# Kernel optimization log

Measured on AMD Instinct MI355X. Metric: run time of the kernel, lower is better.

The kernel has to match this reference:

```python
import jax, jax.numpy as jnp
import numpy as np

N_COMPRESS = 512
N_EXPAND_QK = 512
N_EXPAND_V = 512
TOPK_C, TOPK_QK, TOPK_V = 8, 4, 6


def setup_inputs() -> dict:
    key = jax.random.key(0)
    k1, k2, k3 = jax.random.split(key, 3)
    B, S, D, DS = 4, 4096, 2048, 64
    N = N_COMPRESS + N_EXPAND_QK + N_EXPAND_V
    x = jax.random.normal(k1, (B, S, D), dtype=jnp.float32)
    importance = jax.random.uniform(k2, (B, S), dtype=jnp.float32)
    W_proj = jax.random.normal(k3, (D, DS), dtype=jnp.float32) * (1.0 / np.sqrt(D))
    b_proj = jnp.zeros((DS,), dtype=jnp.float32)
    neuron_emb = jax.random.normal(jax.random.fold_in(key, 7), (N, DS), dtype=jnp.float32) * 0.02
    return {"x": x, "importance": importance, "W_proj": W_proj, "b_proj": b_proj, "neuron_emb": neuron_emb}


def _topk_sparsify(w, k):
    # w: [B, N]; keep top-k per row, zero the rest, renormalize (matches torch scatter path)
    vals, idx = jax.lax.top_k(w, k)
    B = w.shape[0]
    sparse = jnp.zeros_like(w).at[jnp.arange(B)[:, None], idx].set(vals)
    return sparse / (sparse.sum(axis=-1, keepdims=True) + 1e-8)


def reference(x, importance, W_proj, b_proj, neuron_emb):
    # token projection into unified neuron space
    h = x @ W_proj + b_proj                              # [B, S, d_space]
    emb_n = neuron_emb / jnp.maximum(
        jnp.linalg.norm(neuron_emb, axis=-1, keepdims=True), 1e-12)
    all_logits = jnp.einsum('bsd,nd->bsn', h, emb_n)     # [B, S, N_total]

    c_end = N_COMPRESS
    qk_end = N_COMPRESS + N_EXPAND_QK
    compress_pref = jax.nn.softmax(all_logits[..., :c_end], axis=-1)
    pref_QK = jax.nn.softmax(all_logits[..., c_end:qk_end], axis=-1)  # Q and K share logits (eval mode)
    pref_V = jax.nn.softmax(all_logits[..., qk_end:], axis=-1)

    # importance-weighted pooling over the sequence
    dense_C = jnp.einsum('bs,bsn->bn', importance, compress_pref)
    dense_QK = jnp.einsum('bs,bsn->bn', importance, pref_QK)
    dense_V = jnp.einsum('bs,bsn->bn', importance, pref_V)

    w_C = _topk_sparsify(dense_C, TOPK_C)
    w_Q = _topk_sparsify(dense_QK, TOPK_QK)
    w_K = _topk_sparsify(dense_QK, TOPK_QK)
    w_V = _topk_sparsify(dense_V, TOPK_V)
    return jnp.stack([w_C, w_Q, w_K, w_V], axis=0)       # [4, B, N_group]
```

## Files before the change

### kernel.cpp

```cpp
#include <hip/hip_runtime.h>

#define NTOT 1536
#define DD 2048
#define BB 4
#define SS 4096
#define NBB 42
#define TPB 98
#define NTILE 7

typedef __attribute__((ext_vector_type(8))) short bf16x8;
typedef __attribute__((ext_vector_type(4))) float f32x4;

__device__ __forceinline__ void split1(float v, unsigned short& hi, unsigned short& lo) {
  unsigned u = __float_as_uint(v);
  hi = (unsigned short)(u >> 16);
  float hf = __uint_as_float(u & 0xffff0000u);
  float r = v - hf;
  lo = (unsigned short)(__float_as_uint(r) >> 16);
}

__global__ __launch_bounds__(256) void k_prep_emb(const float* __restrict__ emb,
                                                  short* __restrict__ eH,
                                                  short* __restrict__ eL) {
  int wave = threadIdx.x >> 6;
  int lane = threadIdx.x & 63;
  int n = blockIdx.x * 4 + wave;
  float v = emb[n * 64 + lane];
  float ss = v * v;
#pragma unroll
  for (int off = 32; off; off >>= 1) ss += __shfl_xor(ss, off, 64);
  float nrm = fmaxf(sqrtf(ss), 1e-12f);
  float nv = v / nrm;
  unsigned short hi, lo;
  split1(nv, hi, lo);
  eH[n * 64 + lane] = (short)hi;
  eL[n * 64 + lane] = (short)lo;
}

__global__ __launch_bounds__(256) void k_prepw(const float* __restrict__ W,
                                               short* __restrict__ imgH,
                                               short* __restrict__ imgL) {
  int kt = blockIdx.x;
  for (int idx = threadIdx.x; idx < 4096; idx += 256) {
    int n = idx & 63;
    int q = idx >> 6;
    int p = q >> 3;
    int e = q & 7;
    int s = p ^ (n & 7);
    int k = kt * 64 + s * 8 + e;
    float v = W[k * 64 + n];
    unsigned short hi, lo;
    split1(v, hi, lo);
    int flat = kt * 4096 + n * 64 + p * 8 + e;
    imgH[flat] = (short)hi;
    imgL[flat] = (short)lo;
  }
}

__device__ __forceinline__ void split8(float4 a, float4 b, bf16x8& hi, bf16x8& lo) {
  float v[8] = {a.x, a.y, a.z, a.w, b.x, b.y, b.z, b.w};
#pragma unroll
  for (int i = 0; i < 8; ++i) {
    unsigned u = __float_as_uint(v[i]);
    hi[i] = (short)(u >> 16);
    float hf = __uint_as_float(u & 0xffff0000u);
    float r = v[i] - hf;
    lo[i] = (short)(__float_as_uint(r) >> 16);
  }
}

__global__ __launch_bounds__(128, 3) void k_proj(const float* __restrict__ x,
                                                 const float* __restrict__ imgHf,
                                                 const float* __restrict__ imgLf,
                                                 const float* __restrict__ bias,
                                                 short* __restrict__ hH,
                                                 short* __restrict__ hL) {
  __shared__ float XAs[2][2048];
  __shared__ short BHs[2][4096];
  __shared__ short BLs[2][4096];

  int tid = threadIdx.x;
  int w = tid >> 6;
  int l = tid & 63;
  size_t t0 = (size_t)blockIdx.x * 32;

  int stok = tid >> 4;
  int sslot = tid & 15;

  float4 xr[4], bhr[4], blr[4];
  f32x4 acc[4];
#pragma unroll
  for (int i = 0; i < 4; ++i) acc[i] = (f32x4){0.f, 0.f, 0.f, 0.f};

  const float4* imgH4 = (const float4*)imgHf;
  const float4* imgL4 = (const float4*)imgLf;

#define LOADT(KT)                                                                  \
  {                                                                                \
    _Pragma("unroll") for (int c = 0; c < 4; ++c) {                                \
      int tok = c * 8 + stok;                                                      \
      xr[c] = *(const float4*)(x + (t0 + tok) * DD + (KT) * 64 + sslot * 4);       \
      bhr[c] = imgH4[(KT) * 512 + c * 128 + tid];                                  \
      blr[c] = imgL4[(KT) * 512 + c * 128 + tid];                                  \
    }                                                                              \
  }

#define WRITET(DB)                                                                 \
  {                                                                                \
    _Pragma("unroll") for (int c = 0; c < 4; ++c) {                                \
      int tok = c * 8 + stok;                                                      \
      *(float4*)(&XAs[DB][tok * 64 + ((sslot ^ (tok & 7)) << 2)]) = xr[c];         \
      *(float4*)(&BHs[DB][c * 1024 + tid * 8]) = bhr[c];                           \
      *(float4*)(&BLs[DB][c * 1024 + tid * 8]) = blr[c];                           \
    }                                                                              \
  }

  LOADT(0);
  WRITET(0);
  __syncthreads();

  int db = 0;
  for (int kt = 0; kt < 32; ++kt) {
    if (kt < 31) LOADT(kt + 1);

    int row = w * 16 + (l & 15);
#pragma unroll
    for (int ks = 0; ks < 2; ++ks) {
      int s0 = ks * 8 + (l >> 4) * 2;
      float4 xa = *(const float4*)(&XAs[db][row * 64 + ((s0 ^ (row & 7)) << 2)]);
      float4 xb = *(const float4*)(&XAs[db][row * 64 + (((s0 + 1) ^ (row & 7)) << 2)]);
      bf16x8 ahi, alo;
      split8(xa, xb, ahi, alo);
#pragma unroll
      for (int nf = 0; nf < 4; ++nf) {
        int n = nf * 16 + (l & 15);
        int p = (ks * 4 + (l >> 4)) ^ (n & 7);
        bf16x8 bh = *(const bf16x8*)(&BHs[db][n * 64 + p * 8]);
        bf16x8 bl = *(const bf16x8*)(&BLs[db][n * 64 + p * 8]);
        acc[nf] = __builtin_amdgcn_mfma_f32_16x16x32_bf16(ahi, bh, acc[nf], 0, 0, 0);
        acc[nf] = __builtin_amdgcn_mfma_f32_16x16x32_bf16(alo, bh, acc[nf], 0, 0, 0);
        acc[nf] = __builtin_amdgcn_mfma_f32_16x16x32_bf16(ahi, bl, acc[nf], 0, 0, 0);
      }
    }

    if (kt < 31) WRITET(db ^ 1);
    __syncthreads();
    db ^= 1;
  }

#pragma unroll
  for (int nf = 0; nf < 4; ++nf) {
    int n = nf * 16 + (l & 15);
    float bv = bias[n];
#pragma unroll
    for (int j = 0; j < 4; ++j) {
      size_t tok = t0 + w * 16 + (l >> 4) * 4 + j;
      float v = acc[nf][j] + bv;
      unsigned short hi, lo;
      split1(v, hi, lo);
      hH[tok * 64 + n] = (short)hi;
      hL[tok * 64 + n] = (short)lo;
    }
  }
#undef LOADT
#undef WRITET
}

__global__ __launch_bounds__(512, 2) void k_pref(const short* __restrict__ hH,
                                                 const short* __restrict__ hL,
                                                 const short* __restrict__ eH,
                                                 const short* __restrict__ eL,
                                                 const float* __restrict__ imp,
                                                 float* __restrict__ partials) {
  int bid = blockIdx.x;
  int g = bid / (BB * NBB);
  int rem = bid % (BB * NBB);
  int b = rem / NBB;
  int nb = rem % NBB;
  int tid = threadIdx.x;
  int w = tid >> 6;
  int l = tid & 63;
  int col = l & 15;
  int q = l >> 4;

  __shared__ short BLs[4 * 2 * 512 * 8];
  __shared__ float zred[2][8][16];

  bf16x8 BH[4][2];
  {
    const short* eHg = eH + ((size_t)(g * 512 + w * 64 + col)) * 64 + q * 8;
    const short* eLg = eL + ((size_t)(g * 512 + w * 64 + col)) * 64 + q * 8;
#pragma unroll
    for (int nf = 0; nf < 4; ++nf) {
#pragma unroll
      for (int ks = 0; ks < 2; ++ks) {
        BH[nf][ks] = *(const bf16x8*)(eHg + nf * 1024 + ks * 32);
        bf16x8 blv = *(const bf16x8*)(eLg + nf * 1024 + ks * 32);
        *(bf16x8*)(&BLs[((nf * 2 + ks) * 512 + tid) * 8]) = blv;
      }
    }
  }
  __syncthreads();

  int s0 = nb * TPB;
  int slim = s0 + TPB; if (slim > SS) slim = SS;
  float wsum[4] = {0.f, 0.f, 0.f, 0.f};
  int par = 0;

#pragma unroll 1
  for (int tile = 0; tile < NTILE; ++tile) {
    int tbase = s0 + tile * 16;
    int arow = tbase + col; if (arow > SS - 1) arow = SS - 1;
    size_t hoff = ((size_t)b * SS + arow) * 64;
    bf16x8 AH0 = *(const bf16x8*)(hH + hoff + q * 8);
    bf16x8 AH1 = *(const bf16x8*)(hH + hoff + 32 + q * 8);
    bf16x8 AL0 = *(const bf16x8*)(hL + hoff + q * 8);
    bf16x8 AL1 = *(const bf16x8*)(hL + hoff + 32 + q * 8);

    f32x4 acc[4];
#pragma unroll
    for (int nf = 0; nf < 4; ++nf) acc[nf] = (f32x4){0.f, 0.f, 0.f, 0.f};
#pragma unroll
    for (int nf = 0; nf < 4; ++nf) {
      bf16x8 bl0 = *(const bf16x8*)(&BLs[((nf * 2 + 0) * 512 + tid) * 8]);
      bf16x8 bl1 = *(const bf16x8*)(&BLs[((nf * 2 + 1) * 512 + tid) * 8]);
      acc[nf] = __builtin_amdgcn_mfma_f32_16x16x32_bf16(AH0, BH[nf][0], acc[nf], 0, 0, 0);
      acc[nf] = __builtin_amdgcn_mfma_f32_16x16x32_bf16(AL0, BH[nf][0], acc[nf], 0, 0, 0);
      acc[nf] = __builtin_amdgcn_mfma_f32_16x16x32_bf16(AH0, bl0, acc[nf], 0, 0, 0);
      acc[nf] = __builtin_amdgcn_mfma_f32_16x16x32_bf16(AH1, BH[nf][1], acc[nf], 0, 0, 0);
      acc[nf] = __builtin_amdgcn_mfma_f32_16x16x32_bf16(AL1, BH[nf][1], acc[nf], 0, 0, 0);
      acc[nf] = __builtin_amdgcn_mfma_f32_16x16x32_bf16(AH1, bl1, acc[nf], 0, 0, 0);
    }

    float zp[4];
#pragma unroll
    for (int j = 0; j < 4; ++j) {
      zp[j] = __expf(acc[0][j]) + __expf(acc[1][j]) +
              __expf(acc[2][j]) + __expf(acc[3][j]);
    }
#pragma unroll
    for (int off = 1; off <= 8; off <<= 1) {
#pragma unroll
      for (int j = 0; j < 4; ++j) zp[j] += __shfl_xor(zp[j], off, 64);
    }
    float zw = (col == 0) ? zp[0] : (col == 1) ? zp[1] : (col == 2) ? zp[2] : zp[3];
    if (col < 4) zred[par][w][q * 4 + col] = zw;
    __syncthreads();
    float r0, r1, r2, r3;
    {
#pragma unroll
      for (int j = 0; j < 4; ++j) {
        int t16 = q * 4 + j;
        float Z = 0.f;
#pragma unroll
        for (int ww = 0; ww < 8; ++ww) Z += zred[par][ww][t16];
        int s = tbase + t16;
        float iv = (s < slim) ? imp[(size_t)b * SS + s] : 0.f;
        float r = iv / Z;
        if (j == 0) r0 = r; else if (j == 1) r1 = r; else if (j == 2) r2 = r; else r3 = r;
      }
    }
#pragma unroll
    for (int nf = 0; nf < 4; ++nf) {
      wsum[nf] += __expf(acc[nf][0]) * r0 + __expf(acc[nf][1]) * r1 +
                  __expf(acc[nf][2]) * r2 + __expf(acc[nf][3]) * r3;
    }
    par ^= 1;
  }

#pragma unroll
  for (int nf = 0; nf < 4; ++nf) {
    wsum[nf] += __shfl_xor(wsum[nf], 16, 64);
    wsum[nf] += __shfl_xor(wsum[nf], 32, 64);
  }
  if (q == 0) {
    size_t base = ((size_t)(g * BB + b) * NBB + nb) * 512 + w * 64;
#pragma unroll
    for (int nf = 0; nf < 4; ++nf) partials[base + nf * 16 + col] = wsum[nf];
  }
}

__global__ __launch_bounds__(512) void k_topk(const float* __restrict__ partials,
                                              float* __restrict__ out) {
  int g = blockIdx.x >> 2;
  int b = blockIdx.x & 3;
  int tid = threadIdx.x;
  int wave = tid >> 6, lane = tid & 63;

  __shared__ float lv[8][8];
  __shared__ int li[8][8];

  float dense = 0.f;
  const float* p = partials + (size_t)(g * BB + b) * NBB * 512 + tid;
  for (int nb = 0; nb < NBB; ++nb) dense += p[nb * 512];

  int K = (g == 0) ? 8 : (g == 1) ? 4 : 6;
  float val = dense;
  float ssum = 0.f;
  int sel = 0;
  for (int it = 0; it < K; ++it) {
    float v = val;
    int idx = tid;
#pragma unroll
    for (int off = 32; off; off >>= 1) {
      float ov = __shfl_xor(v, off, 64);
      int oi = __shfl_xor(idx, off, 64);
      if (ov > v || (ov == v && oi < idx)) { v = ov; idx = oi; }
    }
    if (lane == 0) { lv[wave][0] = v; li[wave][0] = idx; }
    __syncthreads();
    float mv = lv[0][0];
    int mi = li[0][0];
#pragma unroll
    for (int ww = 1; ww < 8; ++ww) {
      float wv2 = lv[ww][0];
      int wi = li[ww][0];
      if (wv2 > mv || (wv2 == mv && wi < mi)) { mv = wv2; mi = wi; }
    }
    ssum += mv;
    if (tid == mi) { sel = 1; val = -3.0e38f; }
    __syncthreads();
  }
  float o = sel ? dense / (ssum + 1e-8f) : 0.f;
  int row = (g == 0) ? 0 : (g == 1) ? 1 : 3;
  out[((size_t)row * BB + b) * 512 + tid] = o;
  if (g == 1) out[((size_t)2 * BB + b) * 512 + tid] = o;
}

extern "C" void kernel_launch(void* const* d_in, const int* in_sizes, int n_in,
                              void* d_out, int out_size, void* d_ws, size_t ws_size,
                              hipStream_t stream) {
  const float* x    = (const float*)d_in[0];
  const float* imp  = (const float*)d_in[1];
  const float* W    = (const float*)d_in[2];
  const float* bias = (const float*)d_in[3];
  const float* emb  = (const float*)d_in[4];
  float* out = (float*)d_out;

  char* ws = (char*)d_ws;
  short* imgH     = (short*)(ws + 0);
  short* imgL     = (short*)(ws + 262144);
  short* eH       = (short*)(ws + 524288);
  short* eL       = (short*)(ws + 720896);
  short* hH       = (short*)(ws + 917504);
  short* hL       = (short*)(ws + 3014656);
  float* partials = (float*)(ws + 5111808);

  hipLaunchKernelGGL(k_prep_emb, dim3(384), dim3(256), 0, stream, emb, eH, eL);
  hipLaunchKernelGGL(k_prepw, dim3(32), dim3(256), 0, stream, W, imgH, imgL);
  hipLaunchKernelGGL(k_proj, dim3(512), dim3(128), 0, stream,
                     x, (const float*)imgH, (const float*)imgL, bias, hH, hL);
  hipLaunchKernelGGL(k_pref, dim3(3 * BB * NBB), dim3(512), 0, stream,
                     hH, hL, eH, eL, imp, partials);
  hipLaunchKernelGGL(k_topk, dim3(12), dim3(512), 0, stream, partials, out);
}
```

Baseline: 95.53 us.

## Merge prep kernels, split proj tile across 4 waves, prefetch A tiles in pref

Fuses the embedding-normalize and weight-split prep kernels into one launch to remove a kernel launch. The projection kernel moves from 128 to 256 threads per block, with each of 4 waves computing a 16x32 quadrant instead of 2 waves doing 16x64 each. This is meant to hide more memory latency while keeping the same 32-token tiles. The pref kernel now loads the next tile's h rows into registers before the current tile's MFMAs, overlapping global loads with compute at the cost of extra registers.

```diff
diff --git a/kernel.cpp b/kernel.cpp
--- a/kernel.cpp
+++ b/kernel.cpp
@@ -19,57 +19,47 @@
   lo = (unsigned short)(__float_as_uint(r) >> 16);
 }
 
-__global__ __launch_bounds__(256) void k_prep_emb(const float* __restrict__ emb,
-                                                  short* __restrict__ eH,
-                                                  short* __restrict__ eL) {
-  int wave = threadIdx.x >> 6;
-  int lane = threadIdx.x & 63;
-  int n = blockIdx.x * 4 + wave;
-  float v = emb[n * 64 + lane];
-  float ss = v * v;
-#pragma unroll
-  for (int off = 32; off; off >>= 1) ss += __shfl_xor(ss, off, 64);
-  float nrm = fmaxf(sqrtf(ss), 1e-12f);
-  float nv = v / nrm;
-  unsigned short hi, lo;
-  split1(nv, hi, lo);
-  eH[n * 64 + lane] = (short)hi;
-  eL[n * 64 + lane] = (short)lo;
-}
-
-__global__ __launch_bounds__(256) void k_prepw(const float* __restrict__ W,
-                                               short* __restrict__ imgH,
-                                               short* __restrict__ imgL) {
-  int kt = blockIdx.x;
-  for (int idx = threadIdx.x; idx < 4096; idx += 256) {
-    int n = idx & 63;
-    int q = idx >> 6;
-    int p = q >> 3;
-    int e = q & 7;
-    int s = p ^ (n & 7);
-    int k = kt * 64 + s * 8 + e;
-    float v = W[k * 64 + n];
+__global__ __launch_bounds__(256) void k_prep(const float* __restrict__ emb,
+                                              const float* __restrict__ W,
+                                              short* __restrict__ eH,
+                                              short* __restrict__ eL,
+                                              short* __restrict__ imgH,
+                                              short* __restrict__ imgL) {
+  int bid = blockIdx.x;
+  if (bid < 384) {
+    int wave = threadIdx.x >> 6;
+    int lane = threadIdx.x & 63;
+    int n = bid * 4 + wave;
+    float v = emb[n * 64 + lane];
+    float ss = v * v;
+#pragma unroll
+    for (int off = 32; off; off >>= 1) ss += __shfl_xor(ss, off, 64);
+    float nrm = fmaxf(sqrtf(ss), 1e-12f);
+    float nv = v / nrm;
     unsigned short hi, lo;
-    split1(v, hi, lo);
-    int flat = kt * 4096 + n * 64 + p * 8 + e;
-    imgH[flat] = (short)hi;
-    imgL[flat] = (short)lo;
-  }
-}
-
-__device__ __forceinline__ void split8(float4 a, float4 b, bf16x8& hi, bf16x8& lo) {
-  float v[8] = {a.x, a.y, a.z, a.w, b.x, b.y, b.z, b.w};
-#pragma unroll
-  for (int i = 0; i < 8; ++i) {
-    unsigned u = __float_as_uint(v[i]);
-    hi[i] = (short)(u >> 16);
-    float hf = __uint_as_float(u & 0xffff0000u);
-    float r = v[i] - hf;
-    lo[i] = (short)(__float_as_uint(r) >> 16);
-  }
-}
-
-__global__ __launch_bounds__(128, 3) void k_proj(const float* __restrict__ x,
+    split1(nv, hi, lo);
+    eH[n * 64 + lane] = (short)hi;
+    eL[n * 64 + lane] = (short)lo;
+  } else {
+    int kt = bid - 384;
+    for (int idx = threadIdx.x; idx < 4096; idx += 256) {
+      int n = idx & 63;
+      int q = idx >> 6;
+      int p = q >> 3;
+      int e = q & 7;
+      int s = p ^ (n & 7);
+      int k = kt * 64 + s * 8 + e;
+      float v = W[k * 64 + n];
+      unsigned short hi, lo;
+      split1(v, hi, lo);
+      int flat = kt * 4096 + n * 64 + p * 8 + e;
+      imgH[flat] = (short)hi;
+      imgL[flat] = (short)lo;
+    }
+  }
+}
+
+__global__ __launch_bounds__(256, 2) void k_proj(const float* __restrict__ x,
                                                  const float* __restrict__ imgHf,
                                                  const float* __restrict__ imgLf,
                                                  const float* __restrict__ bias,
@@ -84,34 +74,37 @@
   int l = tid & 63;
   size_t t0 = (size_t)blockIdx.x * 32;
 
-  int stok = tid >> 4;
+  int ty = tid >> 4;
   int sslot = tid & 15;
 
-  float4 xr[4], bhr[4], blr[4];
-  f32x4 acc[4];
-#pragma unroll
-  for (int i = 0; i < 4; ++i) acc[i] = (f32x4){0.f, 0.f, 0.f, 0.f};
+  int th = (w & 1) * 16;
+  int nh = (w >> 1) * 32;
+
+  float4 xr[2], bhr[2], blr[2];
+  f32x4 acc[2];
+#pragma unroll
+  for (int i = 0; i < 2; ++i) acc[i] = (f32x4){0.f, 0.f, 0.f, 0.f};
 
   const float4* imgH4 = (const float4*)imgHf;
   const float4* imgL4 = (const float4*)imgLf;
 
 #define LOADT(KT)                                                                  \
   {                                                                                \
-    _Pragma("unroll") for (int c = 0; c < 4; ++c) {                                \
-      int tok = c * 8 + stok;                                                      \
+    _Pragma("unroll") for (int c = 0; c < 2; ++c) {                                \
+      int tok = c * 16 + ty;                                                       \
       xr[c] = *(const float4*)(x + (t0 + tok) * DD + (KT) * 64 + sslot * 4);       \
-      bhr[c] = imgH4[(KT) * 512 + c * 128 + tid];                                  \
-      blr[c] = imgL4[(KT) * 512 + c * 128 + tid];                                  \
+      bhr[c] = imgH4[(KT) * 512 + c * 256 + tid];                                  \
+      blr[c] = imgL4[(KT) * 512 + c * 256 + tid];                                  \
     }                                                                              \
   }
 
 #define WRITET(DB)                                                                 \
   {                                                                                \
-    _Pragma("unroll") for (int c = 0; c < 4; ++c) {                                \
-      int tok = c * 8 + stok;                                                      \
+    _Pragma("unroll") for (int c = 0; c < 2; ++c) {                                \
+      int tok = c * 16 + ty;                                                       \
       *(float4*)(&XAs[DB][tok * 64 + ((sslot ^ (tok & 7)) << 2)]) = xr[c];         \
-      *(float4*)(&BHs[DB][c * 1024 + tid * 8]) = bhr[c];                           \
-      *(float4*)(&BLs[DB][c * 1024 + tid * 8]) = blr[c];                           \
+      *(float4*)(&BHs[DB][(c * 256 + tid) * 8]) = bhr[c];                          \
+      *(float4*)(&BLs[DB][(c * 256 + tid) * 8]) = blr[c];                          \
     }                                                                              \
   }
 
@@ -123,17 +116,27 @@
   for (int kt = 0; kt < 32; ++kt) {
     if (kt < 31) LOADT(kt + 1);
 
-    int row = w * 16 + (l & 15);
+    int row = th + (l & 15);
 #pragma unroll
     for (int ks = 0; ks < 2; ++ks) {
       int s0 = ks * 8 + (l >> 4) * 2;
       float4 xa = *(const float4*)(&XAs[db][row * 64 + ((s0 ^ (row & 7)) << 2)]);
       float4 xb = *(const float4*)(&XAs[db][row * 64 + (((s0 + 1) ^ (row & 7)) << 2)]);
       bf16x8 ahi, alo;
-      split8(xa, xb, ahi, alo);
-#pragma unroll
-      for (int nf = 0; nf < 4; ++nf) {
-        int n = nf * 16 + (l & 15);
+      {
+        float v[8] = {xa.x, xa.y, xa.z, xa.w, xb.x, xb.y, xb.z, xb.w};
+#pragma unroll
+        for (int i = 0; i < 8; ++i) {
+          unsigned u = __float_as_uint(v[i]);
+          ahi[i] = (short)(u >> 16);
+          float hf = __uint_as_float(u & 0xffff0000u);
+          float r = v[i] - hf;
+          alo[i] = (short)(__float_as_uint(r) >> 16);
+        }
+      }
+#pragma unroll
+      for (int nf = 0; nf < 2; ++nf) {
+        int n = nh + nf * 16 + (l & 15);
         int p = (ks * 4 + (l >> 4)) ^ (n & 7);
         bf16x8 bh = *(const bf16x8*)(&BHs[db][n * 64 + p * 8]);
         bf16x8 bl = *(const bf16x8*)(&BLs[db][n * 64 + p * 8]);
@@ -149,12 +152,12 @@
   }
 
 #pragma unroll
-  for (int nf = 0; nf < 4; ++nf) {
-    int n = nf * 16 + (l & 15);
+  for (int nf = 0; nf < 2; ++nf) {
+    int n = nh + nf * 16 + (l & 15);
     float bv = bias[n];
 #pragma unroll
     for (int j = 0; j < 4; ++j) {
-      size_t tok = t0 + w * 16 + (l >> 4) * 4 + j;
+      size_t tok = t0 + th + (l >> 4) * 4 + j;
       float v = acc[nf][j] + bv;
       unsigned short hi, lo;
       split1(v, hi, lo);
@@ -207,15 +210,23 @@
   float wsum[4] = {0.f, 0.f, 0.f, 0.f};
   int par = 0;
 
+#define LOADA(TB, A0, A1, A2, A3)                                        \
+  {                                                                      \
+    int arow = (TB) + col; if (arow > SS - 1) arow = SS - 1;             \
+    size_t hoff = ((size_t)b * SS + arow) * 64;                          \
+    A0 = *(const bf16x8*)(hH + hoff + q * 8);                            \
+    A1 = *(const bf16x8*)(hH + hoff + 32 + q * 8);                       \
+    A2 = *(const bf16x8*)(hL + hoff + q * 8);                            \
+    A3 = *(const bf16x8*)(hL + hoff + 32 + q * 8);                       \
+  }
+
+  bf16x8 AH0, AH1, AL0, AL1, nH0, nH1, nL0, nL1;
+  LOADA(s0, AH0, AH1, AL0, AL1);
+
 #pragma unroll 1
   for (int tile = 0; tile < NTILE; ++tile) {
     int tbase = s0 + tile * 16;
-    int arow = tbase + col; if (arow > SS - 1) arow = SS - 1;
-    size_t hoff = ((size_t)b * SS + arow) * 64;
-    bf16x8 AH0 = *(const bf16x8*)(hH + hoff + q * 8);
-    bf16x8 AH1 = *(const bf16x8*)(hH + hoff + 32 + q * 8);
-    bf16x8 AL0 = *(const bf16x8*)(hL + hoff + q * 8);
-    bf16x8 AL1 = *(const bf16x8*)(hL + hoff + 32 + q * 8);
+    if (tile < NTILE - 1) LOADA(tbase + 16, nH0, nH1, nL0, nL1);
 
     f32x4 acc[4];
 #pragma unroll
@@ -265,8 +276,10 @@
       wsum[nf] += __expf(acc[nf][0]) * r0 + __expf(acc[nf][1]) * r1 +
                   __expf(acc[nf][2]) * r2 + __expf(acc[nf][3]) * r3;
     }
+    AH0 = nH0; AH1 = nH1; AL0 = nL0; AL1 = nL1;
     par ^= 1;
   }
+#undef LOADA
 
 #pragma unroll
   for (int nf = 0; nf < 4; ++nf) {
@@ -346,9 +359,8 @@
   short* hL       = (short*)(ws + 3014656);
   float* partials = (float*)(ws + 5111808);
 
-  hipLaunchKernelGGL(k_prep_emb, dim3(384), dim3(256), 0, stream, emb, eH, eL);
-  hipLaunchKernelGGL(k_prepw, dim3(32), dim3(256), 0, stream, W, imgH, imgL);
-  hipLaunchKernelGGL(k_proj, dim3(512), dim3(128), 0, stream,
+  hipLaunchKernelGGL(k_prep, dim3(416), dim3(256), 0, stream, emb, W, eH, eL, imgH, imgL);
+  hipLaunchKernelGGL(k_proj, dim3(512), dim3(256), 0, stream,
                      x, (const float*)imgH, (const float*)imgL, bias, hH, hL);
   hipLaunchKernelGGL(k_pref, dim3(3 * BB * NBB), dim3(512), 0, stream,
                      hH, hL, eH, eL, imp, partials);
```

Result: faster. 90.30 us (-5.5%).
